# Performance work log

Hardware: AMD Instinct MI355X
Metric: run time of the kernel (lower is better)

## Reference

```python
import jax, jax.numpy as jnp
import numpy as np

N_HEAD = 16
EPS = 1e-6


def setup_inputs() -> dict:
    key = jax.random.key(0)
    k1, k2, k3 = jax.random.split(key, 3)
    B, T, C = 2, 2048, 1024
    x = jax.random.normal(k1, (B, T, C), dtype=jnp.float32)
    w_attn = jax.random.normal(k2, (C, 3 * C), dtype=jnp.float32) * 0.02
    w_proj = jax.random.normal(k3, (C, C), dtype=jnp.float32) * 0.02
    return {"x": x, "w_attn": w_attn, "w_proj": w_proj}


def _linear_attention(q, k, v):
    """q,k,v: (T,B,H,D) with q,k already feature-mapped (elu+1).
    Causal linear attention via a D x D running-state recurrence (same math
    as cumsum of k-v outer products, computed without the O(T*D^2) tensor)."""
    B, H, D = q.shape[1], q.shape[2], q.shape[3]

    def step(carry, qkv_t):
        S, z = carry                      # S:(B,H,D,D), z:(B,H,D)
        qt, kt, vt = qkv_t                # each (B,H,D)
        S = S + kt[..., :, None] * vt[..., None, :]
        z = z + kt
        num = jnp.einsum('bhi,bhij->bhj', qt, S)
        den = jnp.sum(qt * z, axis=-1, keepdims=True)
        return (S, z), num / (den + EPS)

    S0 = jnp.zeros((B, H, D, D), q.dtype)
    z0 = jnp.zeros((B, H, D), q.dtype)
    _, y = jax.lax.scan(step, (S0, z0), (q, k, v))
    return y                              # (T,B,H,D)


def reference(x, w_attn, w_proj):
    B, T, C = x.shape
    H = N_HEAD
    D = C // H
    qkv = x @ w_attn                      # (B,T,3C)
    q, k, v = jnp.split(qkv, 3, axis=-1)

    def to_tbhd(a):                       # (B,T,C) -> (T,B,H,D)
        return a.reshape(B, T, H, D).transpose(1, 0, 2, 3)

    q = jax.nn.elu(to_tbhd(q)) + 1.0      # phi(x) = ELU(x)+1
    k = jax.nn.elu(to_tbhd(k)) + 1.0
    v = to_tbhd(v)

    y = _linear_attention(q, k, v)        # (T,B,H,D)
    y = y.transpose(1, 0, 2, 3).reshape(B, T, C)
    return y @ w_proj                     # resid dropout p=0.0 is identity
```

## Files before the change

kernel.cpp:

```cpp
#include <hip/hip_runtime.h>
#include <hip/hip_bf16.h>
#include <cmath>

#define TB   2048
#define CCH  1024
#define NCH  32
#define EPSF 1e-6f

typedef unsigned short u16;
typedef __attribute__((ext_vector_type(8))) short  frag8;
typedef __attribute__((ext_vector_type(4))) float  floatx4;

__device__ __forceinline__ u16 f2bf(float f) {
    unsigned int u = __float_as_uint(f);
    unsigned int r = (u + 0x7fffu + ((u >> 16) & 1u)) >> 16;
    return (u16)r;
}
__device__ __forceinline__ float bf2f(u16 v) {
    return __uint_as_float(((unsigned int)v) << 16);
}

__device__ __forceinline__ void async_load16(const u16* g, u16* l) {
    __builtin_amdgcn_global_load_lds(
        (const __attribute__((address_space(1))) void*)g,
        (__attribute__((address_space(3))) void*)l,
        16, 0, 0);
}

__global__ __launch_bounds__(256) void prep_k(
    const float* __restrict__ x, const float* __restrict__ wa,
    const float* __restrict__ wp,
    u16* __restrict__ xb, u16* __restrict__ waT, u16* __restrict__ wpT)
{
    __shared__ u16 t[64][65];
    int blk = blockIdx.x;
    if (blk < 2048) {
        int i = (blk * 256 + threadIdx.x) * 8;
        float4 a = *(const float4*)(x + i);
        float4 b = *(const float4*)(x + i + 4);
        u16 v[8];
        v[0] = f2bf(a.x); v[1] = f2bf(a.y); v[2] = f2bf(a.z); v[3] = f2bf(a.w);
        v[4] = f2bf(b.x); v[5] = f2bf(b.y); v[6] = f2bf(b.z); v[7] = f2bf(b.w);
        *(uint4*)(xb + i) = *(uint4*)v;
        return;
    }
    const float* in; u16* out; int K, N, bx, by;
    if (blk < 2048 + 768) {
        int tb = blk - 2048; in = wa; out = waT; K = 1024; N = 3072;
        bx = tb % 48; by = tb / 48;
    } else {
        int tb = blk - 2816; in = wp; out = wpT; K = 1024; N = 1024;
        bx = tb & 15; by = tb >> 4;
    }
    const int k0 = by * 64, n0 = bx * 64;
    const int c = threadIdx.x & 63, r0 = threadIdx.x >> 6;
    for (int r = r0; r < 64; r += 4)
        t[c][r] = f2bf(in[(size_t)(k0 + r) * N + n0 + c]);
    __syncthreads();
    for (int r = r0; r < 64; r += 4)
        out[(size_t)(n0 + r) * K + k0 + c] = t[r][c];
}

__global__ __launch_bounds__(256) void gemm_bf16_bf16out_k(
    const u16* __restrict__ A, const u16* __restrict__ BT,
    u16* __restrict__ C, int N, int K, int phi_cols)
{
    __shared__ u16 Als[128 * 64];
    __shared__ u16 Bls[128 * 64];
    const int tid  = threadIdx.x;
    const int wave = tid >> 6, lane = tid & 63;
    const int quad = lane >> 4, lrow = lane & 15;
    const int wm = wave >> 1, wn = wave & 1;
    const int row0 = blockIdx.y * 128, col0 = blockIdx.x * 128;
    const int lr = lane >> 3;
    const int lc = ((lane & 7) ^ lr) * 8;
    const int rsw = lrow & 7;
    floatx4 acc[4][4] = {};

    for (int k0 = 0; k0 < K; k0 += 64) {
        __syncthreads();
        #pragma unroll
        for (int m = 0; m < 4; ++m) {
            int i = wave * 4 + m;
            async_load16(A  + (size_t)(row0 + i * 8 + lr) * K + k0 + lc, &Als[i * 512]);
            async_load16(BT + (size_t)(col0 + i * 8 + lr) * K + k0 + lc, &Bls[i * 512]);
        }
        __syncthreads();
        #pragma unroll
        for (int ksi = 0; ksi < 2; ++ksi) {
            frag8 af[4], bf[4];
            #pragma unroll
            for (int i = 0; i < 4; ++i)
                af[i] = *(const frag8*)&Als[(wm * 64 + i * 16 + lrow) * 64
                                            + ((ksi * 4 + quad) ^ rsw) * 8];
            #pragma unroll
            for (int i = 0; i < 4; ++i)
                bf[i] = *(const frag8*)&Bls[(wn * 64 + i * 16 + lrow) * 64
                                            + ((ksi * 4 + quad) ^ rsw) * 8];
            #pragma unroll
            for (int i = 0; i < 4; ++i)
                #pragma unroll
                for (int jn = 0; jn < 4; ++jn)
                    acc[i][jn] = __builtin_amdgcn_mfma_f32_16x16x32_bf16(
                        af[i], bf[jn], acc[i][jn], 0, 0, 0);
        }
    }

    #pragma unroll
    for (int i = 0; i < 4; ++i) {
        #pragma unroll
        for (int jn = 0; jn < 4; ++jn) {
            int col = col0 + wn * 64 + jn * 16 + lrow;
            bool isphi = col < phi_cols;
            #pragma unroll
            for (int r = 0; r < 4; ++r) {
                int row = row0 + wm * 64 + i * 16 + quad * 4 + r;
                float v = acc[i][jn][r];
                if (isphi) v = (v > 0.f) ? (v + 1.f) : __expf(v);
                C[(size_t)row * N + col] = f2bf(v);
            }
        }
    }
}

__global__ __launch_bounds__(256) void gemm_bf16_f32out_k(
    const u16* __restrict__ A, const u16* __restrict__ BT,
    float* __restrict__ C, int N, int K)
{
    __shared__ u16 Als[128 * 64];
    __shared__ u16 Bls[64 * 64];
    const int tid  = threadIdx.x;
    const int wave = tid >> 6, lane = tid & 63;
    const int quad = lane >> 4, lrow = lane & 15;
    const int wm = wave >> 1, wn = wave & 1;
    const int row0 = blockIdx.y * 128, col0 = blockIdx.x * 64;
    const int lr = lane >> 3;
    const int lc = ((lane & 7) ^ lr) * 8;
    const int rsw = lrow & 7;
    floatx4 acc[4][2] = {};

    for (int k0 = 0; k0 < K; k0 += 64) {
        __syncthreads();
        #pragma unroll
        for (int m = 0; m < 4; ++m) {
            int i = wave * 4 + m;
            async_load16(A + (size_t)(row0 + i * 8 + lr) * K + k0 + lc, &Als[i * 512]);
        }
        #pragma unroll
        for (int m = 0; m < 2; ++m) {
            int i = wave * 2 + m;
            async_load16(BT + (size_t)(col0 + i * 8 + lr) * K + k0 + lc, &Bls[i * 512]);
        }
        __syncthreads();
        #pragma unroll
        for (int ksi = 0; ksi < 2; ++ksi) {
            frag8 af[4], bf[2];
            #pragma unroll
            for (int i = 0; i < 4; ++i)
                af[i] = *(const frag8*)&Als[(wm * 64 + i * 16 + lrow) * 64
                                            + ((ksi * 4 + quad) ^ rsw) * 8];
            #pragma unroll
            for (int jn = 0; jn < 2; ++jn)
                bf[jn] = *(const frag8*)&Bls[(wn * 32 + jn * 16 + lrow) * 64
                                             + ((ksi * 4 + quad) ^ rsw) * 8];
            #pragma unroll
            for (int i = 0; i < 4; ++i)
                #pragma unroll
                for (int jn = 0; jn < 2; ++jn)
                    acc[i][jn] = __builtin_amdgcn_mfma_f32_16x16x32_bf16(
                        af[i], bf[jn], acc[i][jn], 0, 0, 0);
        }
    }

    #pragma unroll
    for (int i = 0; i < 4; ++i)
        #pragma unroll
        for (int jn = 0; jn < 2; ++jn) {
            int col = col0 + wn * 32 + jn * 16 + lrow;
            #pragma unroll
            for (int r = 0; r < 4; ++r) {
                int row = row0 + wm * 64 + i * 16 + quad * 4 + r;
                C[(size_t)row * N + col] = acc[i][jn][r];
            }
        }
}

__global__ __launch_bounds__(256) void chunk_kv_mfma_k(
    const u16* __restrict__ qkv,
    u16* __restrict__ Spt,
    float* __restrict__ zloc)
{
    __shared__ u16 Kt[64][72];
    __shared__ u16 Vt[64][72];
    const int tid  = threadIdx.x;
    const int wave = tid >> 6, lane = tid & 63;
    const int quad = lane >> 4, lrow = lane & 15;
    const int blk = blockIdx.x;
    const int c = blk & 31, h = (blk >> 5) & 15, b = blk >> 9;
    const int t0 = c * 64;
    const u16* base = qkv + (size_t)(b * TB + t0) * 3072 + h * 64;

    #pragma unroll
    for (int m = 0; m < 2; ++m) {
        int chunk = tid + 256 * m;
        int s = chunk >> 3, d0 = (chunk & 7) * 8;
        const u16* row = base + (size_t)s * 3072;
        u16 kv[8], vv[8];
        *(uint4*)kv = *(const uint4*)(row + 1024 + d0);
        *(uint4*)vv = *(const uint4*)(row + 2048 + d0);
        #pragma unroll
        for (int q = 0; q < 8; ++q) { Kt[d0 + q][s] = kv[q]; Vt[d0 + q][s] = vv[q]; }
    }
    __syncthreads();

    frag8 vf[2];
    #pragma unroll
    for (int ks = 0; ks < 2; ++ks)
        vf[ks] = *(const frag8*)&Vt[wave * 16 + lrow][ks * 32 + quad * 8];
    u16* So = Spt + (size_t)blk * 4096;
    #pragma unroll
    for (int jn = 0; jn < 4; ++jn) {
        floatx4 acc = {};
        #pragma unroll
        for (int ks = 0; ks < 2; ++ks) {
            frag8 kf = *(const frag8*)&Kt[jn * 16 + lrow][ks * 32 + quad * 8];
            acc = __builtin_amdgcn_mfma_f32_16x16x32_bf16(vf[ks], kf, acc, 0, 0, 0);
        }
        #pragma unroll
        for (int r = 0; r < 4; ++r) {
            int j = wave * 16 + quad * 4 + r;
            int i = jn * 16 + lrow;
            So[j * 64 + i] = f2bf(acc[r]);
        }
    }
    if (tid < 64) {
        float z = 0.f;
        for (int s = 0; s < 64; ++s) z += bf2f(Kt[tid][s]);
        zloc[(size_t)blk * 64 + tid] = z;
    }
}

__global__ __launch_bounds__(256) void scan_state_k(
    u16* __restrict__ Spt, float* __restrict__ z)
{
    const int bh = blockIdx.x >> 1;
    const int part = blockIdx.x & 1;
    const int e0 = part * 2048 + threadIdx.x * 8;
    const size_t base = (size_t)bh * NCH * 4096;
    float r[8] = {};
    for (int c = 0; c < NCH; ++c) {
        u16* p = Spt + base + (size_t)c * 4096 + e0;
        u16 t[8];
        *(uint4*)t = *(const uint4*)p;
        u16 o[8];
        #pragma unroll
        for (int q = 0; q < 8; ++q) { o[q] = f2bf(r[q]); r[q] += bf2f(t[q]); }
        *(uint4*)p = *(uint4*)o;
    }
    if (part == 0 && threadIdx.x < 64) {
        const size_t zb = (size_t)bh * NCH * 64;
        float rz = 0.f;
        for (int c = 0; c < NCH; ++c) {
            float t = z[zb + c * 64 + threadIdx.x];
            z[zb + c * 64 + threadIdx.x] = rz;
            rz += t;
        }
    }
}

__global__ __launch_bounds__(256) void attn_mfma_k(
    const u16* __restrict__ qkv,
    const u16* __restrict__ SptG,
    const float* __restrict__ zp,
    u16* __restrict__ Yb)
{
    __shared__ u16 Qs[64][72];
    __shared__ u16 Ks[64][72];
    __shared__ u16 Vt[64][72];
    __shared__ u16 Sp[64][72];
    __shared__ float zps[64];
    __shared__ float den4[64][4];
    __shared__ float den[64];

    const int tid  = threadIdx.x;
    const int wave = tid >> 6, lane = tid & 63;
    const int quad = lane >> 4, lrow = lane & 15;
    const int blk = blockIdx.x;
    const int c = blk & 31, h = (blk >> 5) & 15, b = blk >> 9;
    const int t0 = c * 64;
    const u16* base = qkv + (size_t)(b * TB + t0) * 3072 + h * 64;

    #pragma unroll
    for (int m = 0; m < 2; ++m) {
        int chunk = tid + 256 * m;
        int s = chunk >> 3, d0 = (chunk & 7) * 8;
        const u16* row = base + (size_t)s * 3072;
        *(uint4*)&Qs[s][d0] = *(const uint4*)(row + d0);
        *(uint4*)&Ks[s][d0] = *(const uint4*)(row + 1024 + d0);
        u16 vv[8];
        *(uint4*)vv = *(const uint4*)(row + 2048 + d0);
        #pragma unroll
        for (int q = 0; q < 8; ++q) Vt[d0 + q][s] = vv[q];
        *(uint4*)&Sp[s][d0] = *(const uint4*)(SptG + (size_t)blk * 4096 + chunk * 8);
    }
    if (tid < 64) zps[tid] = zp[(size_t)blk * 64 + tid];
    __syncthreads();

    frag8 qf[2];
    #pragma unroll
    for (int ks = 0; ks < 2; ++ks)
        qf[ks] = *(const frag8*)&Qs[wave * 16 + lrow][ks * 32 + quad * 8];

    floatx4 yacc[4] = {}, kacc[4] = {};
    #pragma unroll
    for (int jn = 0; jn < 4; ++jn) {
        #pragma unroll
        for (int ks = 0; ks < 2; ++ks) {
            frag8 spf = *(const frag8*)&Sp[jn * 16 + lrow][ks * 32 + quad * 8];
            yacc[jn] = __builtin_amdgcn_mfma_f32_16x16x32_bf16(qf[ks], spf, yacc[jn], 0, 0, 0);
            frag8 kf = *(const frag8*)&Ks[jn * 16 + lrow][ks * 32 + quad * 8];
            kacc[jn] = __builtin_amdgcn_mfma_f32_16x16x32_bf16(qf[ks], kf, kacc[jn], 0, 0, 0);
        }
    }
    __syncthreads();

    #pragma unroll
    for (int jn = 0; jn < 4; ++jn) {
        int s = jn * 16 + lrow;
        #pragma unroll
        for (int r = 0; r < 4; ++r) {
            int t = wave * 16 + quad * 4 + r;
            float v = (s <= t) ? kacc[jn][r] : 0.f;
            Sp[t][s] = f2bf(v);
        }
    }
    __syncthreads();

    {
        int t = tid >> 2, seg = tid & 3;
        float p = 0.f;
        #pragma unroll
        for (int i = 0; i < 16; ++i) {
            int d = seg * 16 + i;
            p += bf2f(Qs[t][d]) * zps[d] + bf2f(Sp[t][d]);
        }
        den4[t][seg] = p;
    }

    frag8 af2[2];
    #pragma unroll
    for (int ks = 0; ks < 2; ++ks)
        af2[ks] = *(const frag8*)&Sp[wave * 16 + lrow][ks * 32 + quad * 8];
    #pragma unroll
    for (int jn = 0; jn < 4; ++jn)
        #pragma unroll
        for (int ks = 0; ks < 2; ++ks) {
            frag8 vf = *(const frag8*)&Vt[jn * 16 + lrow][ks * 32 + quad * 8];
            yacc[jn] = __builtin_amdgcn_mfma_f32_16x16x32_bf16(af2[ks], vf, yacc[jn], 0, 0, 0);
        }
    __syncthreads();
    if (tid < 64) den[tid] = den4[tid][0] + den4[tid][1] + den4[tid][2] + den4[tid][3];
    __syncthreads();

    #pragma unroll
    for (int jn = 0; jn < 4; ++jn) {
        #pragma unroll
        for (int r = 0; r < 4; ++r) {
            int t = wave * 16 + quad * 4 + r;
            float inv = 1.f / (den[t] + EPSF);
            Qs[t][jn * 16 + lrow] = f2bf(yacc[jn][r] * inv);
        }
    }
    __syncthreads();
    {
        int row = tid >> 2, seg = tid & 3;
        size_t o = (size_t)(b * TB + t0 + row) * CCH + h * 64 + seg * 16;
        *(uint4*)(Yb + o)     = *(uint4*)&Qs[row][seg * 16];
        *(uint4*)(Yb + o + 8) = *(uint4*)&Qs[row][seg * 16 + 8];
    }
}

extern "C" void kernel_launch(void* const* d_in, const int* in_sizes, int n_in,
                              void* d_out, int out_size, void* d_ws, size_t ws_size,
                              hipStream_t stream)
{
    const float* x      = (const float*)d_in[0];
    const float* w_attn = (const float*)d_in[1];
    const float* w_proj = (const float*)d_in[2];
    float* out = (float*)d_out;

    u16* xb    = (u16*)d_ws;
    u16* waT   = xb    + (size_t)4096 * 1024;
    u16* wpT   = waT   + (size_t)3072 * 1024;
    u16* Yb    = wpT   + (size_t)1024 * 1024;
    u16* qkv_b = Yb    + (size_t)4096 * 1024;
    u16* Spt   = qkv_b + (size_t)4096 * 3072;
    float* zloc = (float*)(Spt + (size_t)1024 * 4096);

    prep_k<<<3072, 256, 0, stream>>>(x, w_attn, w_proj, xb, waT, wpT);

    gemm_bf16_bf16out_k<<<dim3(24, 32), 256, 0, stream>>>(xb, waT, qkv_b, 3072, 1024, 2048);

    chunk_kv_mfma_k<<<1024, 256, 0, stream>>>(qkv_b, Spt, zloc);
    scan_state_k   <<<64,   256, 0, stream>>>(Spt, zloc);
    attn_mfma_k    <<<1024, 256, 0, stream>>>(qkv_b, Spt, zloc, Yb);

    gemm_bf16_f32out_k<<<dim3(16, 32), 256, 0, stream>>>(Yb, wpT, out, 1024, 1024);
}
```

Measured before the change: 172.1 us.

## Fuse chunk-state, scan, and attention kernels into one cooperative kernel with grid syncs

Merges the three linear-attention stages (per-chunk KV state, prefix scan over chunks, intra-chunk attention) into a single cooperative kernel of 512 blocks. Each block handles two chunks per phase, and the phases are separated by grid.sync(). The aim is to remove two kernel launches and their inter-kernel gaps. In exchange it adds grid-wide barrier cost, and only 64 of 512 blocks do work during the serial scan phase while the rest sit idle.

```diff
diff --git a/kernel.cpp b/kernel.cpp
--- a/kernel.cpp
+++ b/kernel.cpp
@@ -1,6 +1,9 @@
 #include <hip/hip_runtime.h>
 #include <hip/hip_bf16.h>
+#include <hip/hip_cooperative_groups.h>
 #include <cmath>
+
+namespace cg = cooperative_groups;
 
 #define TB   2048
 #define CCH  1024
@@ -185,93 +188,10 @@
         }
 }
 
-__global__ __launch_bounds__(256) void chunk_kv_mfma_k(
+__global__ __launch_bounds__(256) void attn_fused_k(
     const u16* __restrict__ qkv,
     u16* __restrict__ Spt,
-    float* __restrict__ zloc)
-{
-    __shared__ u16 Kt[64][72];
-    __shared__ u16 Vt[64][72];
-    const int tid  = threadIdx.x;
-    const int wave = tid >> 6, lane = tid & 63;
-    const int quad = lane >> 4, lrow = lane & 15;
-    const int blk = blockIdx.x;
-    const int c = blk & 31, h = (blk >> 5) & 15, b = blk >> 9;
-    const int t0 = c * 64;
-    const u16* base = qkv + (size_t)(b * TB + t0) * 3072 + h * 64;
-
-    #pragma unroll
-    for (int m = 0; m < 2; ++m) {
-        int chunk = tid + 256 * m;
-        int s = chunk >> 3, d0 = (chunk & 7) * 8;
-        const u16* row = base + (size_t)s * 3072;
-        u16 kv[8], vv[8];
-        *(uint4*)kv = *(const uint4*)(row + 1024 + d0);
-        *(uint4*)vv = *(const uint4*)(row + 2048 + d0);
-        #pragma unroll
-        for (int q = 0; q < 8; ++q) { Kt[d0 + q][s] = kv[q]; Vt[d0 + q][s] = vv[q]; }
-    }
-    __syncthreads();
-
-    frag8 vf[2];
-    #pragma unroll
-    for (int ks = 0; ks < 2; ++ks)
-        vf[ks] = *(const frag8*)&Vt[wave * 16 + lrow][ks * 32 + quad * 8];
-    u16* So = Spt + (size_t)blk * 4096;
-    #pragma unroll
-    for (int jn = 0; jn < 4; ++jn) {
-        floatx4 acc = {};
-        #pragma unroll
-        for (int ks = 0; ks < 2; ++ks) {
-            frag8 kf = *(const frag8*)&Kt[jn * 16 + lrow][ks * 32 + quad * 8];
-            acc = __builtin_amdgcn_mfma_f32_16x16x32_bf16(vf[ks], kf, acc, 0, 0, 0);
-        }
-        #pragma unroll
-        for (int r = 0; r < 4; ++r) {
-            int j = wave * 16 + quad * 4 + r;
-            int i = jn * 16 + lrow;
-            So[j * 64 + i] = f2bf(acc[r]);
-        }
-    }
-    if (tid < 64) {
-        float z = 0.f;
-        for (int s = 0; s < 64; ++s) z += bf2f(Kt[tid][s]);
-        zloc[(size_t)blk * 64 + tid] = z;
-    }
-}
-
-__global__ __launch_bounds__(256) void scan_state_k(
-    u16* __restrict__ Spt, float* __restrict__ z)
-{
-    const int bh = blockIdx.x >> 1;
-    const int part = blockIdx.x & 1;
-    const int e0 = part * 2048 + threadIdx.x * 8;
-    const size_t base = (size_t)bh * NCH * 4096;
-    float r[8] = {};
-    for (int c = 0; c < NCH; ++c) {
-        u16* p = Spt + base + (size_t)c * 4096 + e0;
-        u16 t[8];
-        *(uint4*)t = *(const uint4*)p;
-        u16 o[8];
-        #pragma unroll
-        for (int q = 0; q < 8; ++q) { o[q] = f2bf(r[q]); r[q] += bf2f(t[q]); }
-        *(uint4*)p = *(uint4*)o;
-    }
-    if (part == 0 && threadIdx.x < 64) {
-        const size_t zb = (size_t)bh * NCH * 64;
-        float rz = 0.f;
-        for (int c = 0; c < NCH; ++c) {
-            float t = z[zb + c * 64 + threadIdx.x];
-            z[zb + c * 64 + threadIdx.x] = rz;
-            rz += t;
-        }
-    }
-}
-
-__global__ __launch_bounds__(256) void attn_mfma_k(
-    const u16* __restrict__ qkv,
-    const u16* __restrict__ SptG,
-    const float* __restrict__ zp,
+    float* __restrict__ zloc,
     u16* __restrict__ Yb)
 {
     __shared__ u16 Qs[64][72];
@@ -285,98 +205,176 @@
     const int tid  = threadIdx.x;
     const int wave = tid >> 6, lane = tid & 63;
     const int quad = lane >> 4, lrow = lane & 15;
-    const int blk = blockIdx.x;
-    const int c = blk & 31, h = (blk >> 5) & 15, b = blk >> 9;
-    const int t0 = c * 64;
-    const u16* base = qkv + (size_t)(b * TB + t0) * 3072 + h * 64;
-
-    #pragma unroll
-    for (int m = 0; m < 2; ++m) {
-        int chunk = tid + 256 * m;
-        int s = chunk >> 3, d0 = (chunk & 7) * 8;
-        const u16* row = base + (size_t)s * 3072;
-        *(uint4*)&Qs[s][d0] = *(const uint4*)(row + d0);
-        *(uint4*)&Ks[s][d0] = *(const uint4*)(row + 1024 + d0);
-        u16 vv[8];
-        *(uint4*)vv = *(const uint4*)(row + 2048 + d0);
-        #pragma unroll
-        for (int q = 0; q < 8; ++q) Vt[d0 + q][s] = vv[q];
-        *(uint4*)&Sp[s][d0] = *(const uint4*)(SptG + (size_t)blk * 4096 + chunk * 8);
-    }
-    if (tid < 64) zps[tid] = zp[(size_t)blk * 64 + tid];
-    __syncthreads();
-
-    frag8 qf[2];
-    #pragma unroll
-    for (int ks = 0; ks < 2; ++ks)
-        qf[ks] = *(const frag8*)&Qs[wave * 16 + lrow][ks * 32 + quad * 8];
-
-    floatx4 yacc[4] = {}, kacc[4] = {};
-    #pragma unroll
-    for (int jn = 0; jn < 4; ++jn) {
-        #pragma unroll
-        for (int ks = 0; ks < 2; ++ks) {
-            frag8 spf = *(const frag8*)&Sp[jn * 16 + lrow][ks * 32 + quad * 8];
-            yacc[jn] = __builtin_amdgcn_mfma_f32_16x16x32_bf16(qf[ks], spf, yacc[jn], 0, 0, 0);
-            frag8 kf = *(const frag8*)&Ks[jn * 16 + lrow][ks * 32 + quad * 8];
-            kacc[jn] = __builtin_amdgcn_mfma_f32_16x16x32_bf16(qf[ks], kf, kacc[jn], 0, 0, 0);
-        }
-    }
-    __syncthreads();
-
-    #pragma unroll
-    for (int jn = 0; jn < 4; ++jn) {
-        int s = jn * 16 + lrow;
-        #pragma unroll
-        for (int r = 0; r < 4; ++r) {
-            int t = wave * 16 + quad * 4 + r;
-            float v = (s <= t) ? kacc[jn][r] : 0.f;
-            Sp[t][s] = f2bf(v);
-        }
-    }
-    __syncthreads();
-
-    {
-        int t = tid >> 2, seg = tid & 3;
-        float p = 0.f;
-        #pragma unroll
-        for (int i = 0; i < 16; ++i) {
-            int d = seg * 16 + i;
-            p += bf2f(Qs[t][d]) * zps[d] + bf2f(Sp[t][d]);
-        }
-        den4[t][seg] = p;
-    }
-
-    frag8 af2[2];
-    #pragma unroll
-    for (int ks = 0; ks < 2; ++ks)
-        af2[ks] = *(const frag8*)&Sp[wave * 16 + lrow][ks * 32 + quad * 8];
-    #pragma unroll
-    for (int jn = 0; jn < 4; ++jn)
-        #pragma unroll
-        for (int ks = 0; ks < 2; ++ks) {
-            frag8 vf = *(const frag8*)&Vt[jn * 16 + lrow][ks * 32 + quad * 8];
-            yacc[jn] = __builtin_amdgcn_mfma_f32_16x16x32_bf16(af2[ks], vf, yacc[jn], 0, 0, 0);
-        }
-    __syncthreads();
-    if (tid < 64) den[tid] = den4[tid][0] + den4[tid][1] + den4[tid][2] + den4[tid][3];
-    __syncthreads();
-
-    #pragma unroll
-    for (int jn = 0; jn < 4; ++jn) {
-        #pragma unroll
-        for (int r = 0; r < 4; ++r) {
-            int t = wave * 16 + quad * 4 + r;
-            float inv = 1.f / (den[t] + EPSF);
-            Qs[t][jn * 16 + lrow] = f2bf(yacc[jn][r] * inv);
-        }
-    }
-    __syncthreads();
-    {
-        int row = tid >> 2, seg = tid & 3;
-        size_t o = (size_t)(b * TB + t0 + row) * CCH + h * 64 + seg * 16;
-        *(uint4*)(Yb + o)     = *(uint4*)&Qs[row][seg * 16];
-        *(uint4*)(Yb + o + 8) = *(uint4*)&Qs[row][seg * 16 + 8];
+    cg::grid_group grid = cg::this_grid();
+
+    #pragma unroll 1
+    for (int half = 0; half < 2; ++half) {
+        const int blk = blockIdx.x * 2 + half;
+        const int c = blk & 31, h = (blk >> 5) & 15, b = blk >> 9;
+        const u16* base = qkv + (size_t)(b * TB + c * 64) * 3072 + h * 64;
+
+        #pragma unroll
+        for (int m = 0; m < 2; ++m) {
+            int chunk = tid + 256 * m;
+            int s = chunk >> 3, d0 = (chunk & 7) * 8;
+            const u16* row = base + (size_t)s * 3072;
+            u16 kv[8], vv[8];
+            *(uint4*)kv = *(const uint4*)(row + 1024 + d0);
+            *(uint4*)vv = *(const uint4*)(row + 2048 + d0);
+            #pragma unroll
+            for (int q = 0; q < 8; ++q) { Sp[d0 + q][s] = kv[q]; Vt[d0 + q][s] = vv[q]; }
+        }
+        __syncthreads();
+
+        frag8 vf[2];
+        #pragma unroll
+        for (int ks = 0; ks < 2; ++ks)
+            vf[ks] = *(const frag8*)&Vt[wave * 16 + lrow][ks * 32 + quad * 8];
+        u16* So = Spt + (size_t)blk * 4096;
+        #pragma unroll
+        for (int jn = 0; jn < 4; ++jn) {
+            floatx4 acc = {};
+            #pragma unroll
+            for (int ks = 0; ks < 2; ++ks) {
+                frag8 kf = *(const frag8*)&Sp[jn * 16 + lrow][ks * 32 + quad * 8];
+                acc = __builtin_amdgcn_mfma_f32_16x16x32_bf16(vf[ks], kf, acc, 0, 0, 0);
+            }
+            #pragma unroll
+            for (int r = 0; r < 4; ++r)
+                So[(wave * 16 + quad * 4 + r) * 64 + jn * 16 + lrow] = f2bf(acc[r]);
+        }
+        if (tid < 64) {
+            float z = 0.f;
+            for (int s = 0; s < 64; ++s) z += bf2f(Sp[tid][s]);
+            zloc[(size_t)blk * 64 + tid] = z;
+        }
+        __syncthreads();
+    }
+    grid.sync();
+
+    if (blockIdx.x < 64) {
+        const int bh = blockIdx.x >> 1;
+        const int part = blockIdx.x & 1;
+        const int e0 = part * 2048 + tid * 8;
+        const size_t sbase = (size_t)bh * NCH * 4096;
+        float r[8] = {};
+        for (int c = 0; c < NCH; ++c) {
+            u16* p = Spt + sbase + (size_t)c * 4096 + e0;
+            u16 t[8];
+            *(uint4*)t = *(const uint4*)p;
+            u16 o[8];
+            #pragma unroll
+            for (int q = 0; q < 8; ++q) { o[q] = f2bf(r[q]); r[q] += bf2f(t[q]); }
+            *(uint4*)p = *(uint4*)o;
+        }
+        if (part == 0 && tid < 64) {
+            const size_t zb = (size_t)bh * NCH * 64;
+            float rz = 0.f;
+            for (int c = 0; c < NCH; ++c) {
+                float t = zloc[zb + c * 64 + tid];
+                zloc[zb + c * 64 + tid] = rz;
+                rz += t;
+            }
+        }
+    }
+    grid.sync();
+
+    #pragma unroll 1
+    for (int half = 0; half < 2; ++half) {
+        const int blk = blockIdx.x * 2 + half;
+        const int c = blk & 31, h = (blk >> 5) & 15, b = blk >> 9;
+        const int t0 = c * 64;
+        const u16* base = qkv + (size_t)(b * TB + t0) * 3072 + h * 64;
+
+        #pragma unroll
+        for (int m = 0; m < 2; ++m) {
+            int chunk = tid + 256 * m;
+            int s = chunk >> 3, d0 = (chunk & 7) * 8;
+            const u16* row = base + (size_t)s * 3072;
+            *(uint4*)&Qs[s][d0] = *(const uint4*)(row + d0);
+            *(uint4*)&Ks[s][d0] = *(const uint4*)(row + 1024 + d0);
+            u16 vv[8];
+            *(uint4*)vv = *(const uint4*)(row + 2048 + d0);
+            #pragma unroll
+            for (int q = 0; q < 8; ++q) Vt[d0 + q][s] = vv[q];
+            *(uint4*)&Sp[s][d0] = *(const uint4*)(Spt + (size_t)blk * 4096 + chunk * 8);
+        }
+        if (tid < 64) zps[tid] = zloc[(size_t)blk * 64 + tid];
+        __syncthreads();
+
+        frag8 qf[2];
+        #pragma unroll
+        for (int ks = 0; ks < 2; ++ks)
+            qf[ks] = *(const frag8*)&Qs[wave * 16 + lrow][ks * 32 + quad * 8];
+
+        floatx4 yacc[4] = {}, kacc[4] = {};
+        #pragma unroll
+        for (int jn = 0; jn < 4; ++jn) {
+            #pragma unroll
+            for (int ks = 0; ks < 2; ++ks) {
+                frag8 spf = *(const frag8*)&Sp[jn * 16 + lrow][ks * 32 + quad * 8];
+                yacc[jn] = __builtin_amdgcn_mfma_f32_16x16x32_bf16(qf[ks], spf, yacc[jn], 0, 0, 0);
+                frag8 kf = *(const frag8*)&Ks[jn * 16 + lrow][ks * 32 + quad * 8];
+                kacc[jn] = __builtin_amdgcn_mfma_f32_16x16x32_bf16(qf[ks], kf, kacc[jn], 0, 0, 0);
+            }
+        }
+        __syncthreads();
+
+        #pragma unroll
+        for (int jn = 0; jn < 4; ++jn) {
+            int s = jn * 16 + lrow;
+            #pragma unroll
+            for (int r = 0; r < 4; ++r) {
+                int t = wave * 16 + quad * 4 + r;
+                float v = (s <= t) ? kacc[jn][r] : 0.f;
+                Sp[t][s] = f2bf(v);
+            }
+        }
+        __syncthreads();
+
+        {
+            int t = tid >> 2, seg = tid & 3;
+            float p = 0.f;
+            #pragma unroll
+            for (int i = 0; i < 16; ++i) {
+                int d = seg * 16 + i;
+                p += bf2f(Qs[t][d]) * zps[d] + bf2f(Sp[t][d]);
+            }
+            den4[t][seg] = p;
+        }
+
+        frag8 af2[2];
+        #pragma unroll
+        for (int ks = 0; ks < 2; ++ks)
+            af2[ks] = *(const frag8*)&Sp[wave * 16 + lrow][ks * 32 + quad * 8];
+        #pragma unroll
+        for (int jn = 0; jn < 4; ++jn)
+            #pragma unroll
+            for (int ks = 0; ks < 2; ++ks) {
+                frag8 vf = *(const frag8*)&Vt[jn * 16 + lrow][ks * 32 + quad * 8];
+                yacc[jn] = __builtin_amdgcn_mfma_f32_16x16x32_bf16(af2[ks], vf, yacc[jn], 0, 0, 0);
+            }
+        __syncthreads();
+        if (tid < 64) den[tid] = den4[tid][0] + den4[tid][1] + den4[tid][2] + den4[tid][3];
+        __syncthreads();
+
+        #pragma unroll
+        for (int jn = 0; jn < 4; ++jn) {
+            #pragma unroll
+            for (int r = 0; r < 4; ++r) {
+                int t = wave * 16 + quad * 4 + r;
+                float inv = 1.f / (den[t] + EPSF);
+                Qs[t][jn * 16 + lrow] = f2bf(yacc[jn][r] * inv);
+            }
+        }
+        __syncthreads();
+        {
+            int row = tid >> 2, seg = tid & 3;
+            size_t o = (size_t)(b * TB + t0 + row) * CCH + h * 64 + seg * 16;
+            *(uint4*)(Yb + o)     = *(uint4*)&Qs[row][seg * 16];
+            *(uint4*)(Yb + o + 8) = *(uint4*)&Qs[row][seg * 16 + 8];
+        }
+        __syncthreads();
     }
 }
 
@@ -401,9 +399,11 @@
 
     gemm_bf16_bf16out_k<<<dim3(24, 32), 256, 0, stream>>>(xb, waT, qkv_b, 3072, 1024, 2048);
 
-    chunk_kv_mfma_k<<<1024, 256, 0, stream>>>(qkv_b, Spt, zloc);
-    scan_state_k   <<<64,   256, 0, stream>>>(Spt, zloc);
-    attn_mfma_k    <<<1024, 256, 0, stream>>>(qkv_b, Spt, zloc, Yb);
+    {
+        void* args[] = { (void*)&qkv_b, (void*)&Spt, (void*)&zloc, (void*)&Yb };
+        hipLaunchCooperativeKernel((const void*)attn_fused_k,
+                                   dim3(512), dim3(256), args, 0, stream);
+    }
 
     gemm_bf16_f32out_k<<<dim3(16, 32), 256, 0, stream>>>(Yb, wpT, out, 1024, 1024);
 }
```

New measurement: 305.1 us. 77.3% more time.

## Fuse chunk-state prefix scan into attention kernel by recomputing prefix sums

Applied to the files above, without the earlier changes.

Removes the separate scan_state_k launch and instead has each attention block sum the per-chunk KV states of all preceding chunks directly from global memory. This eliminates a poorly parallel 64-block kernel and its read-modify-write pass over the state buffer. In exchange, total reads grow quadratically with chunk count (about 16x more state loads on average), and late chunks do serial work that unbalances the blocks.

```diff
diff --git a/kernel.cpp b/kernel.cpp
--- a/kernel.cpp
+++ b/kernel.cpp
@@ -240,38 +240,10 @@
     }
 }
 
-__global__ __launch_bounds__(256) void scan_state_k(
-    u16* __restrict__ Spt, float* __restrict__ z)
-{
-    const int bh = blockIdx.x >> 1;
-    const int part = blockIdx.x & 1;
-    const int e0 = part * 2048 + threadIdx.x * 8;
-    const size_t base = (size_t)bh * NCH * 4096;
-    float r[8] = {};
-    for (int c = 0; c < NCH; ++c) {
-        u16* p = Spt + base + (size_t)c * 4096 + e0;
-        u16 t[8];
-        *(uint4*)t = *(const uint4*)p;
-        u16 o[8];
-        #pragma unroll
-        for (int q = 0; q < 8; ++q) { o[q] = f2bf(r[q]); r[q] += bf2f(t[q]); }
-        *(uint4*)p = *(uint4*)o;
-    }
-    if (part == 0 && threadIdx.x < 64) {
-        const size_t zb = (size_t)bh * NCH * 64;
-        float rz = 0.f;
-        for (int c = 0; c < NCH; ++c) {
-            float t = z[zb + c * 64 + threadIdx.x];
-            z[zb + c * 64 + threadIdx.x] = rz;
-            rz += t;
-        }
-    }
-}
-
 __global__ __launch_bounds__(256) void attn_mfma_k(
     const u16* __restrict__ qkv,
     const u16* __restrict__ SptG,
-    const float* __restrict__ zp,
+    const float* __restrict__ zloc,
     u16* __restrict__ Yb)
 {
     __shared__ u16 Qs[64][72];
@@ -301,9 +273,30 @@
         *(uint4*)vv = *(const uint4*)(row + 2048 + d0);
         #pragma unroll
         for (int q = 0; q < 8; ++q) Vt[d0 + q][s] = vv[q];
-        *(uint4*)&Sp[s][d0] = *(const uint4*)(SptG + (size_t)blk * 4096 + chunk * 8);
-    }
-    if (tid < 64) zps[tid] = zp[(size_t)blk * 64 + tid];
+    }
+
+    {
+        const u16* Sbase = SptG + (size_t)(blk - c) * 4096;
+        const int e0 = tid * 16;
+        float a16[16] = {};
+        for (int cc = 0; cc < c; ++cc) {
+            const u16* p = Sbase + (size_t)cc * 4096 + e0;
+            u16 t[16];
+            *(uint4*)t       = *(const uint4*)p;
+            *(uint4*)(t + 8) = *(const uint4*)(p + 8);
+            #pragma unroll
+            for (int q = 0; q < 16; ++q) a16[q] += bf2f(t[q]);
+        }
+        int row = tid >> 2, col = (tid & 3) * 16;
+        #pragma unroll
+        for (int q = 0; q < 16; ++q) Sp[row][col + q] = f2bf(a16[q]);
+        if (tid < 64) {
+            const float* zb = zloc + (size_t)(blk - c) * 64;
+            float rz = 0.f;
+            for (int cc = 0; cc < c; ++cc) rz += zb[cc * 64 + tid];
+            zps[tid] = rz;
+        }
+    }
     __syncthreads();
 
     frag8 qf[2];
@@ -402,7 +395,6 @@
     gemm_bf16_bf16out_k<<<dim3(24, 32), 256, 0, stream>>>(xb, waT, qkv_b, 3072, 1024, 2048);
 
     chunk_kv_mfma_k<<<1024, 256, 0, stream>>>(qkv_b, Spt, zloc);
-    scan_state_k   <<<64,   256, 0, stream>>>(Spt, zloc);
     attn_mfma_k    <<<1024, 256, 0, stream>>>(qkv_b, Spt, zloc, Yb);
 
     gemm_bf16_f32out_k<<<dim3(16, 32), 256, 0, stream>>>(Yb, wpT, out, 1024, 1024);
```

Result: slower. 178.0 us (+3.4%).
